# Optimization experiments

Hardware: AMD Instinct MI355X
Metric: run time of the kernel (lower is better)

## Reference

```python
import jax, jax.numpy as jnp
import numpy as np

S, B, D = 2048, 32, 1024
H = 16
DIM = D // H  # 64 per-head dim
EPS = 1e-5


def setup_inputs() -> dict:
    key = jax.random.key(0)
    k1, k2, k3 = jax.random.split(key, 3)
    src = jax.random.normal(k1, (S, B, D), dtype=jnp.float32)
    # per-head bracket Linear(2*dim -> dim), stacked over heads
    bound = 1.0 / np.sqrt(2 * DIM)
    W = jax.random.uniform(k2, (H, 2 * DIM, DIM), minval=-bound, maxval=bound, dtype=jnp.float32)
    b = jax.random.uniform(k3, (H, DIM), minval=-bound, maxval=bound, dtype=jnp.float32)
    # shared LayerNorm(d_model) params (default init: gamma=1, beta=0)
    gamma = jnp.ones((D,), dtype=jnp.float32)
    beta = jnp.zeros((D,), dtype=jnp.float32)
    return {"src": src, "W": W, "b": b, "gamma": gamma, "beta": beta}


def reference(src, W, b, gamma, beta):
    def layer_norm(x):
        mu = jnp.mean(x, axis=-1, keepdims=True)
        var = jnp.mean(jnp.square(x - mu), axis=-1, keepdims=True)
        return (x - mu) * jax.lax.rsqrt(var + EPS) * gamma + beta

    def step(c, x):
        # c, x: [B, D]; mode='base': y_h = GELU(Linear_h([c_h; x_h])), new context = x
        ch = c.reshape(B, H, DIM)
        xh = x.reshape(B, H, DIM)
        cat = jnp.concatenate([ch, xh], axis=-1)              # [B, H, 2*DIM]
        y = jax.nn.gelu(jnp.einsum('bhk,hkd->bhd', cat, W) + b, approximate=False)
        c_new = layer_norm(x)                                  # LN(context)=LN(x)
        y_out = layer_norm(y.reshape(B, D))
        return c_new, y_out

    c0 = jnp.zeros((B, D), dtype=src.dtype)
    _, ys = jax.lax.scan(step, c0, src)
    return ys  # [S, B, D]
```

## Files before the change

### kernel.cpp

```cpp
#include <hip/hip_runtime.h>

#define SS 2048
#define BB 32
#define DD 1024
#define HH 16
#define RB 8

typedef unsigned short u16;
typedef unsigned int u32;
using f32x4 = __attribute__((ext_vector_type(4))) float;
using bf16x8 = __attribute__((ext_vector_type(8))) short;

__device__ __forceinline__ u16 f2bf(float x) {
  union { float f; u32 u; } c; c.f = x;
  u32 r = c.u + 0x7fffu + ((c.u >> 16) & 1u);
  return (u16)(r >> 16);
}
__device__ __forceinline__ int swzb(int row, int col) {
  return ((row << 11) + (col << 1)) ^ ((row & 7) << 4);
}
__device__ __forceinline__ void st_lds8(u16* base, int row, int col,
                                        float4 a, float4 b) {
  uint4 pk;
  pk.x = (u32)f2bf(a.x) | ((u32)f2bf(a.y) << 16);
  pk.y = (u32)f2bf(a.z) | ((u32)f2bf(a.w) << 16);
  pk.z = (u32)f2bf(b.x) | ((u32)f2bf(b.y) << 16);
  pk.w = (u32)f2bf(b.z) | ((u32)f2bf(b.w) << 16);
  *reinterpret_cast<uint4*>(reinterpret_cast<char*>(base) + swzb(row, col)) = pk;
}
__device__ __forceinline__ void st_lds8z(u16* base, int row, int col) {
  uint4 pk; pk.x = pk.y = pk.z = pk.w = 0u;
  *reinterpret_cast<uint4*>(reinterpret_cast<char*>(base) + swzb(row, col)) = pk;
}
__device__ __forceinline__ bf16x8 ld_afrag(const u16* base, int row, int col) {
  return *reinterpret_cast<const bf16x8*>(reinterpret_cast<const char*>(base) + swzb(row, col));
}
__device__ __forceinline__ float gelu_f(float v) {
  const float u2 = 1.5957691216057308f * v * __builtin_fmaf(0.044715f, v * v, 1.0f);
  const float e = __expf(u2);
  const float th = 1.0f - 2.0f * __builtin_amdgcn_rcpf(e + 1.0f);
  return 0.5f * v * (1.0f + th);
}

__global__ void prep_w(const float* __restrict__ W, u16* __restrict__ Wf) {
  const int o = blockIdx.x * 256 + threadIdx.x;
  const int l = o & 63;
  const int tile = o >> 6;
  const int nt = tile & 3, ks = (tile >> 2) & 3, h = tile >> 4;
  const int d = nt * 16 + (l & 15);
  const int kb = ks * 32 + 8 * (l >> 4);
  u16 v[8];
#pragma unroll
  for (int j = 0; j < 8; ++j) v[j] = f2bf(W[(h * 128 + kb + j) * 64 + d]);
  uint4 pk;
  pk.x = (u32)v[0] | ((u32)v[1] << 16);
  pk.y = (u32)v[2] | ((u32)v[3] << 16);
  pk.z = (u32)v[4] | ((u32)v[5] << 16);
  pk.w = (u32)v[6] | ((u32)v[7] << 16);
  reinterpret_cast<uint4*>(Wf)[o] = pk;
}

__global__ __launch_bounds__(256, 4) void lienet_main(
    const float* __restrict__ src, const u16* __restrict__ Wf,
    const float* __restrict__ bias, const float* __restrict__ gamma,
    const float* __restrict__ beta, float* __restrict__ out) {
  __shared__ __align__(16) u16 cbuf[RB * DD];
  __shared__ __align__(16) u16 xbuf[RB * DD];
  __shared__ float part[4][RB][2];

  const int bid = blockIdx.x;
  const int lin = (bid & 7) * 1024 + (bid >> 3);
  const int t = lin >> 2;
  const int row0 = (lin & 3) * RB;

  const int tid = threadIdx.x;
  const int wave = tid >> 6;
  const int lane = tid & 63;
  const int c0 = lane * 8;

#pragma unroll
  for (int rr = 0; rr < 2; ++rr) {
    const int row = wave * 2 + rr;
    const int grow = row0 + row;
    {
      const float* rp = src + ((size_t)t * BB + grow) * DD;
      float4 f0 = *reinterpret_cast<const float4*>(rp + c0);
      float4 f1 = *reinterpret_cast<const float4*>(rp + c0 + 4);
      float4 f2 = *reinterpret_cast<const float4*>(rp + 512 + c0);
      float4 f3 = *reinterpret_cast<const float4*>(rp + 512 + c0 + 4);
      st_lds8(xbuf, row, c0, f0, f1);
      st_lds8(xbuf, row, 512 + c0, f2, f3);
    }
    if (t == 0) {
      st_lds8z(cbuf, row, c0);
      st_lds8z(cbuf, row, 512 + c0);
    } else {
      const float* rp = src + ((size_t)(t - 1) * BB + grow) * DD;
      float f[16];
      *reinterpret_cast<float4*>(f + 0) = *reinterpret_cast<const float4*>(rp + c0);
      *reinterpret_cast<float4*>(f + 4) = *reinterpret_cast<const float4*>(rp + c0 + 4);
      *reinterpret_cast<float4*>(f + 8) = *reinterpret_cast<const float4*>(rp + 512 + c0);
      *reinterpret_cast<float4*>(f + 12) = *reinterpret_cast<const float4*>(rp + 512 + c0 + 4);
      float s1 = 0.f, s2 = 0.f;
#pragma unroll
      for (int j = 0; j < 16; ++j) { s1 += f[j]; s2 += f[j] * f[j]; }
#pragma unroll
      for (int off = 32; off; off >>= 1) { s1 += __shfl_xor(s1, off); s2 += __shfl_xor(s2, off); }
      const float mu = s1 * (1.f / 1024.f);
      const float rs = rsqrtf(s2 * (1.f / 1024.f) - mu * mu + 1e-5f);
      float4 g0 = *reinterpret_cast<const float4*>(gamma + c0);
      float4 g1 = *reinterpret_cast<const float4*>(gamma + c0 + 4);
      float4 g2 = *reinterpret_cast<const float4*>(gamma + 512 + c0);
      float4 g3 = *reinterpret_cast<const float4*>(gamma + 512 + c0 + 4);
      float4 b0 = *reinterpret_cast<const float4*>(beta + c0);
      float4 b1 = *reinterpret_cast<const float4*>(beta + c0 + 4);
      float4 b2 = *reinterpret_cast<const float4*>(beta + 512 + c0);
      float4 b3 = *reinterpret_cast<const float4*>(beta + 512 + c0 + 4);
      float4 o0, o1, o2, o3;
      o0.x = (f[0] - mu) * rs * g0.x + b0.x;  o0.y = (f[1] - mu) * rs * g0.y + b0.y;
      o0.z = (f[2] - mu) * rs * g0.z + b0.z;  o0.w = (f[3] - mu) * rs * g0.w + b0.w;
      o1.x = (f[4] - mu) * rs * g1.x + b1.x;  o1.y = (f[5] - mu) * rs * g1.y + b1.y;
      o1.z = (f[6] - mu) * rs * g1.z + b1.z;  o1.w = (f[7] - mu) * rs * g1.w + b1.w;
      o2.x = (f[8] - mu) * rs * g2.x + b2.x;  o2.y = (f[9] - mu) * rs * g2.y + b2.y;
      o2.z = (f[10] - mu) * rs * g2.z + b2.z; o2.w = (f[11] - mu) * rs * g2.w + b2.w;
      o3.x = (f[12] - mu) * rs * g3.x + b3.x; o3.y = (f[13] - mu) * rs * g3.y + b3.y;
      o3.z = (f[14] - mu) * rs * g3.z + b3.z; o3.w = (f[15] - mu) * rs * g3.w + b3.w;
      st_lds8(cbuf, row, c0, o0, o1);
      st_lds8(cbuf, row, 512 + c0, o2, o3);
    }
  }
  __syncthreads();

  f32x4 acc[4][4];
#pragma unroll
  for (int hh = 0; hh < 4; ++hh)
#pragma unroll
    for (int nt = 0; nt < 4; ++nt) acc[hh][nt] = (f32x4){0.f, 0.f, 0.f, 0.f};

  const int arow = lane & 7;
  const int kb = 8 * (lane >> 4);
#pragma unroll
  for (int ks = 0; ks < 4; ++ks) {
    const u16* sb = (ks < 2) ? cbuf : xbuf;
#pragma unroll
    for (int hh = 0; hh < 4; ++hh) {
      const int h = wave * 4 + hh;
      bf16x8 a = ld_afrag(sb, arow, h * 64 + (ks & 1) * 32 + kb);
      const uint4* wp = reinterpret_cast<const uint4*>(Wf) + ((h * 4 + ks) * 4) * 64 + lane;
#pragma unroll
      for (int nt = 0; nt < 4; ++nt) {
        uint4 wv = wp[nt * 64];
        bf16x8 bfr = *reinterpret_cast<bf16x8*>(&wv);
        acc[hh][nt] = __builtin_amdgcn_mfma_f32_16x16x32_bf16(a, bfr, acc[hh][nt], 0, 0, 0);
      }
    }
  }

  const int hilo = lane >> 5;
  const int row4 = 4 * ((lane >> 4) & 1);
  const int cl = lane & 15;
  float gv[2][4][4];
#pragma unroll
  for (int hp = 0; hp < 2; ++hp) {
    const int h_eff = wave * 4 + hp + 2 * hilo;
#pragma unroll
    for (int nt = 0; nt < 4; ++nt) {
      const float bv = bias[h_eff * 64 + nt * 16 + cl];
#pragma unroll
      for (int r = 0; r < 4; ++r) {
        const float v = (hilo ? acc[hp + 2][nt][r] : acc[hp][nt][r]) + bv;
        gv[hp][nt][r] = gelu_f(v);
      }
    }
  }
  float s1[4], s2[4];
#pragma unroll
  for (int r = 0; r < 4; ++r) {
    float a = 0.f, b = 0.f;
#pragma unroll
    for (int hp = 0; hp < 2; ++hp)
#pragma unroll
      for (int nt = 0; nt < 4; ++nt) {
        const float g = gv[hp][nt][r];
        a += g; b += g * g;
      }
    a += __shfl_xor(a, 1); b += __shfl_xor(b, 1);
    a += __shfl_xor(a, 2); b += __shfl_xor(b, 2);
    a += __shfl_xor(a, 4); b += __shfl_xor(b, 4);
    a += __shfl_xor(a, 8); b += __shfl_xor(b, 8);
    a += __shfl_xor(a, 32); b += __shfl_xor(b, 32);
    s1[r] = a; s2[r] = b;
  }
  if (lane == 0 || lane == 16) {
#pragma unroll
    for (int r = 0; r < 4; ++r) {
      part[wave][row4 + r][0] = s1[r];
      part[wave][row4 + r][1] = s2[r];
    }
  }
  float gm[2][4], bt[2][4];
#pragma unroll
  for (int hp = 0; hp < 2; ++hp) {
    const int h_eff = wave * 4 + hp + 2 * hilo;
#pragma unroll
    for (int nt = 0; nt < 4; ++nt) {
      const int dcol = h_eff * 64 + nt * 16 + cl;
      gm[hp][nt] = gamma[dcol];
      bt[hp][nt] = beta[dcol];
    }
  }
  __syncthreads();

  float mu[4], rs[4];
#pragma unroll
  for (int r = 0; r < 4; ++r) {
    const int row = row4 + r;
    const float a = part[0][row][0] + part[1][row][0] + part[2][row][0] + part[3][row][0];
    const float b = part[0][row][1] + part[1][row][1] + part[2][row][1] + part[3][row][1];
    mu[r] = a * (1.f / 1024.f);
    rs[r] = rsqrtf(b * (1.f / 1024.f) - mu[r] * mu[r] + 1e-5f);
  }
#pragma unroll
  for (int hp = 0; hp < 2; ++hp) {
    const int h_eff = wave * 4 + hp + 2 * hilo;
#pragma unroll
    for (int nt = 0; nt < 4; ++nt) {
      const int dcol = h_eff * 64 + nt * 16 + cl;
#pragma unroll
      for (int r = 0; r < 4; ++r) {
        const float o = (gv[hp][nt][r] - mu[r]) * rs[r] * gm[hp][nt] + bt[hp][nt];
        out[((size_t)t * BB + row0 + row4 + r) * DD + dcol] = o;
      }
    }
  }
}

extern "C" void kernel_launch(void* const* d_in, const int* in_sizes, int n_in,
                              void* d_out, int out_size, void* d_ws, size_t ws_size,
                              hipStream_t stream) {
  const float* src = (const float*)d_in[0];
  const float* W = (const float*)d_in[1];
  const float* bias = (const float*)d_in[2];
  const float* gamma = (const float*)d_in[3];
  const float* beta = (const float*)d_in[4];
  float* out = (float*)d_out;
  u16* Wf = (u16*)d_ws;

  prep_w<<<64, 256, 0, stream>>>(W, Wf);
  lienet_main<<<SS * 4, 256, 0, stream>>>(src, Wf, bias, gamma, beta, out);
}
```

Baseline: 228.4 us.

## Process eight timesteps per block, reusing the staged input as next context

Each block now loops over eight consecutive timesteps for sixteen batch rows with 512 threads. The LDS copy of x for step t is turned in place into the LayerNorm context for step t+1, and the next x is prefetched into registers while GELU and the reductions run. This removes the second global read of src for the context and fills all sixteen MFMA rows instead of eight. In exchange the grid shrinks to 512 larger blocks with serial steps and extra barriers. The context LayerNorm is now computed from bf16-rounded x rather than fp32, which slightly changes numerics.

```diff
diff --git a/kernel.cpp b/kernel.cpp
--- a/kernel.cpp
+++ b/kernel.cpp
@@ -3,8 +3,9 @@
 #define SS 2048
 #define BB 32
 #define DD 1024
-#define HH 16
-#define RB 8
+#define RB 16
+#define GT 8
+#define NW 8
 
 typedef unsigned short u16;
 typedef unsigned int u32;
@@ -16,11 +17,13 @@
   u32 r = c.u + 0x7fffu + ((c.u >> 16) & 1u);
   return (u16)(r >> 16);
 }
+__device__ __forceinline__ float bf2f(u32 h) {
+  union { u32 u; float f; } c; c.u = h << 16; return c.f;
+}
 __device__ __forceinline__ int swzb(int row, int col) {
   return ((row << 11) + (col << 1)) ^ ((row & 7) << 4);
 }
-__device__ __forceinline__ void st_lds8(u16* base, int row, int col,
-                                        float4 a, float4 b) {
+__device__ __forceinline__ void st8(u16* base, int row, int col, float4 a, float4 b) {
   uint4 pk;
   pk.x = (u32)f2bf(a.x) | ((u32)f2bf(a.y) << 16);
   pk.y = (u32)f2bf(a.z) | ((u32)f2bf(a.w) << 16);
@@ -28,9 +31,12 @@
   pk.w = (u32)f2bf(b.z) | ((u32)f2bf(b.w) << 16);
   *reinterpret_cast<uint4*>(reinterpret_cast<char*>(base) + swzb(row, col)) = pk;
 }
-__device__ __forceinline__ void st_lds8z(u16* base, int row, int col) {
+__device__ __forceinline__ void st8z(u16* base, int row, int col) {
   uint4 pk; pk.x = pk.y = pk.z = pk.w = 0u;
   *reinterpret_cast<uint4*>(reinterpret_cast<char*>(base) + swzb(row, col)) = pk;
+}
+__device__ __forceinline__ uint4 ld16(const u16* base, int row, int col) {
+  return *reinterpret_cast<const uint4*>(reinterpret_cast<const char*>(base) + swzb(row, col));
 }
 __device__ __forceinline__ bf16x8 ld_afrag(const u16* base, int row, int col) {
   return *reinterpret_cast<const bf16x8*>(reinterpret_cast<const char*>(base) + swzb(row, col));
@@ -40,6 +46,37 @@
   const float e = __expf(u2);
   const float th = 1.0f - 2.0f * __builtin_amdgcn_rcpf(e + 1.0f);
   return 0.5f * v * (1.0f + th);
+}
+
+__device__ __forceinline__ void ln_row_to_c(u16* cbuf, int row, int c0, const float* v,
+                                            const float* __restrict__ gamma,
+                                            const float* __restrict__ beta) {
+  float s1 = 0.f, s2 = 0.f;
+#pragma unroll
+  for (int j = 0; j < 16; ++j) { s1 += v[j]; s2 += v[j] * v[j]; }
+#pragma unroll
+  for (int off = 32; off; off >>= 1) { s1 += __shfl_xor(s1, off); s2 += __shfl_xor(s2, off); }
+  const float mu = s1 * (1.f / 1024.f);
+  const float rs = rsqrtf(s2 * (1.f / 1024.f) - mu * mu + 1e-5f);
+  float4 g0 = *reinterpret_cast<const float4*>(gamma + c0);
+  float4 g1 = *reinterpret_cast<const float4*>(gamma + c0 + 4);
+  float4 g2 = *reinterpret_cast<const float4*>(gamma + 512 + c0);
+  float4 g3 = *reinterpret_cast<const float4*>(gamma + 512 + c0 + 4);
+  float4 b0 = *reinterpret_cast<const float4*>(beta + c0);
+  float4 b1 = *reinterpret_cast<const float4*>(beta + c0 + 4);
+  float4 b2 = *reinterpret_cast<const float4*>(beta + 512 + c0);
+  float4 b3 = *reinterpret_cast<const float4*>(beta + 512 + c0 + 4);
+  float4 o0, o1, o2, o3;
+  o0.x = (v[0] - mu) * rs * g0.x + b0.x;   o0.y = (v[1] - mu) * rs * g0.y + b0.y;
+  o0.z = (v[2] - mu) * rs * g0.z + b0.z;   o0.w = (v[3] - mu) * rs * g0.w + b0.w;
+  o1.x = (v[4] - mu) * rs * g1.x + b1.x;   o1.y = (v[5] - mu) * rs * g1.y + b1.y;
+  o1.z = (v[6] - mu) * rs * g1.z + b1.z;   o1.w = (v[7] - mu) * rs * g1.w + b1.w;
+  o2.x = (v[8] - mu) * rs * g2.x + b2.x;   o2.y = (v[9] - mu) * rs * g2.y + b2.y;
+  o2.z = (v[10] - mu) * rs * g2.z + b2.z;  o2.w = (v[11] - mu) * rs * g2.w + b2.w;
+  o3.x = (v[12] - mu) * rs * g3.x + b3.x;  o3.y = (v[13] - mu) * rs * g3.y + b3.y;
+  o3.z = (v[14] - mu) * rs * g3.z + b3.z;  o3.w = (v[15] - mu) * rs * g3.w + b3.w;
+  st8(cbuf, row, c0, o0, o1);
+  st8(cbuf, row, 512 + c0, o2, o3);
 }
 
 __global__ void prep_w(const float* __restrict__ W, u16* __restrict__ Wf) {
@@ -48,10 +85,10 @@
   const int tile = o >> 6;
   const int nt = tile & 3, ks = (tile >> 2) & 3, h = tile >> 4;
   const int d = nt * 16 + (l & 15);
-  const int kb = ks * 32 + 8 * (l >> 4);
+  const int kbw = ks * 32 + 8 * (l >> 4);
   u16 v[8];
 #pragma unroll
-  for (int j = 0; j < 8; ++j) v[j] = f2bf(W[(h * 128 + kb + j) * 64 + d]);
+  for (int j = 0; j < 8; ++j) v[j] = f2bf(W[(h * 128 + kbw + j) * 64 + d]);
   uint4 pk;
   pk.x = (u32)v[0] | ((u32)v[1] << 16);
   pk.y = (u32)v[2] | ((u32)v[3] << 16);
@@ -60,178 +97,162 @@
   reinterpret_cast<uint4*>(Wf)[o] = pk;
 }
 
-__global__ __launch_bounds__(256, 4) void lienet_main(
+__global__ __launch_bounds__(512, 4) void lienet_main(
     const float* __restrict__ src, const u16* __restrict__ Wf,
     const float* __restrict__ bias, const float* __restrict__ gamma,
     const float* __restrict__ beta, float* __restrict__ out) {
   __shared__ __align__(16) u16 cbuf[RB * DD];
   __shared__ __align__(16) u16 xbuf[RB * DD];
-  __shared__ float part[4][RB][2];
+  __shared__ __align__(16) float part[RB][NW][2];
 
   const int bid = blockIdx.x;
-  const int lin = (bid & 7) * 1024 + (bid >> 3);
-  const int t = lin >> 2;
-  const int row0 = (lin & 3) * RB;
+  const int t0 = (bid >> 1) * GT;
+  const int rg = bid & 1;
 
   const int tid = threadIdx.x;
   const int wave = tid >> 6;
   const int lane = tid & 63;
   const int c0 = lane * 8;
+  const int r0 = wave * 2;
+  const int kb = 8 * (lane >> 4);
+  const int cl = lane & 15;
+  const int rq = lane >> 4;
 
 #pragma unroll
   for (int rr = 0; rr < 2; ++rr) {
-    const int row = wave * 2 + rr;
-    const int grow = row0 + row;
-    {
-      const float* rp = src + ((size_t)t * BB + grow) * DD;
-      float4 f0 = *reinterpret_cast<const float4*>(rp + c0);
-      float4 f1 = *reinterpret_cast<const float4*>(rp + c0 + 4);
-      float4 f2 = *reinterpret_cast<const float4*>(rp + 512 + c0);
-      float4 f3 = *reinterpret_cast<const float4*>(rp + 512 + c0 + 4);
-      st_lds8(xbuf, row, c0, f0, f1);
-      st_lds8(xbuf, row, 512 + c0, f2, f3);
-    }
-    if (t == 0) {
-      st_lds8z(cbuf, row, c0);
-      st_lds8z(cbuf, row, 512 + c0);
+    const int row = r0 + rr;
+    const int grow = rg * RB + row;
+    const float* xp = src + ((size_t)t0 * BB + grow) * DD;
+    float4 xa = *reinterpret_cast<const float4*>(xp + c0);
+    float4 xb = *reinterpret_cast<const float4*>(xp + c0 + 4);
+    float4 xc = *reinterpret_cast<const float4*>(xp + 512 + c0);
+    float4 xd = *reinterpret_cast<const float4*>(xp + 512 + c0 + 4);
+    st8(xbuf, row, c0, xa, xb);
+    st8(xbuf, row, 512 + c0, xc, xd);
+    if (t0 == 0) {
+      st8z(cbuf, row, c0);
+      st8z(cbuf, row, 512 + c0);
     } else {
-      const float* rp = src + ((size_t)(t - 1) * BB + grow) * DD;
-      float f[16];
-      *reinterpret_cast<float4*>(f + 0) = *reinterpret_cast<const float4*>(rp + c0);
-      *reinterpret_cast<float4*>(f + 4) = *reinterpret_cast<const float4*>(rp + c0 + 4);
-      *reinterpret_cast<float4*>(f + 8) = *reinterpret_cast<const float4*>(rp + 512 + c0);
-      *reinterpret_cast<float4*>(f + 12) = *reinterpret_cast<const float4*>(rp + 512 + c0 + 4);
-      float s1 = 0.f, s2 = 0.f;
-#pragma unroll
-      for (int j = 0; j < 16; ++j) { s1 += f[j]; s2 += f[j] * f[j]; }
-#pragma unroll
-      for (int off = 32; off; off >>= 1) { s1 += __shfl_xor(s1, off); s2 += __shfl_xor(s2, off); }
-      const float mu = s1 * (1.f / 1024.f);
-      const float rs = rsqrtf(s2 * (1.f / 1024.f) - mu * mu + 1e-5f);
-      float4 g0 = *reinterpret_cast<const float4*>(gamma + c0);
-      float4 g1 = *reinterpret_cast<const float4*>(gamma + c0 + 4);
-      float4 g2 = *reinterpret_cast<const float4*>(gamma + 512 + c0);
-      float4 g3 = *reinterpret_cast<const float4*>(gamma + 512 + c0 + 4);
-      float4 b0 = *reinterpret_cast<const float4*>(beta + c0);
-      float4 b1 = *reinterpret_cast<const float4*>(beta + c0 + 4);
-      float4 b2 = *reinterpret_cast<const float4*>(beta + 512 + c0);
-      float4 b3 = *reinterpret_cast<const float4*>(beta + 512 + c0 + 4);
-      float4 o0, o1, o2, o3;
-      o0.x = (f[0] - mu) * rs * g0.x + b0.x;  o0.y = (f[1] - mu) * rs * g0.y + b0.y;
-      o0.z = (f[2] - mu) * rs * g0.z + b0.z;  o0.w = (f[3] - mu) * rs * g0.w + b0.w;
-      o1.x = (f[4] - mu) * rs * g1.x + b1.x;  o1.y = (f[5] - mu) * rs * g1.y + b1.y;
-      o1.z = (f[6] - mu) * rs * g1.z + b1.z;  o1.w = (f[7] - mu) * rs * g1.w + b1.w;
-      o2.x = (f[8] - mu) * rs * g2.x + b2.x;  o2.y = (f[9] - mu) * rs * g2.y + b2.y;
-      o2.z = (f[10] - mu) * rs * g2.z + b2.z; o2.w = (f[11] - mu) * rs * g2.w + b2.w;
-      o3.x = (f[12] - mu) * rs * g3.x + b3.x; o3.y = (f[13] - mu) * rs * g3.y + b3.y;
-      o3.z = (f[14] - mu) * rs * g3.z + b3.z; o3.w = (f[15] - mu) * rs * g3.w + b3.w;
-      st_lds8(cbuf, row, c0, o0, o1);
-      st_lds8(cbuf, row, 512 + c0, o2, o3);
+      const float* cp = src + ((size_t)(t0 - 1) * BB + grow) * DD;
+      float v[16];
+      *reinterpret_cast<float4*>(v + 0)  = *reinterpret_cast<const float4*>(cp + c0);
+      *reinterpret_cast<float4*>(v + 4)  = *reinterpret_cast<const float4*>(cp + c0 + 4);
+      *reinterpret_cast<float4*>(v + 8)  = *reinterpret_cast<const float4*>(cp + 512 + c0);
+      *reinterpret_cast<float4*>(v + 12) = *reinterpret_cast<const float4*>(cp + 512 + c0 + 4);
+      ln_row_to_c(cbuf, row, c0, v, gamma, beta);
     }
   }
+  f32x4 acc[2][4];
+#pragma unroll
+  for (int hh = 0; hh < 2; ++hh)
+#pragma unroll
+    for (int nt = 0; nt < 4; ++nt) acc[hh][nt] = (f32x4){0.f, 0.f, 0.f, 0.f};
   __syncthreads();
 
-  f32x4 acc[4][4];
-#pragma unroll
-  for (int hh = 0; hh < 4; ++hh)
-#pragma unroll
-    for (int nt = 0; nt < 4; ++nt) acc[hh][nt] = (f32x4){0.f, 0.f, 0.f, 0.f};
-
-  const int arow = lane & 7;
-  const int kb = 8 * (lane >> 4);
-#pragma unroll
-  for (int ks = 0; ks < 4; ++ks) {
-    const u16* sb = (ks < 2) ? cbuf : xbuf;
-#pragma unroll
-    for (int hh = 0; hh < 4; ++hh) {
-      const int h = wave * 4 + hh;
-      bf16x8 a = ld_afrag(sb, arow, h * 64 + (ks & 1) * 32 + kb);
-      const uint4* wp = reinterpret_cast<const uint4*>(Wf) + ((h * 4 + ks) * 4) * 64 + lane;
+  for (int t = t0; t < t0 + GT; ++t) {
+    __builtin_amdgcn_s_setprio(1);
+#pragma unroll
+    for (int ks = 0; ks < 4; ++ks) {
+      const u16* sb = (ks < 2) ? cbuf : xbuf;
+#pragma unroll
+      for (int hh = 0; hh < 2; ++hh) {
+        const int h = wave * 2 + hh;
+        bf16x8 afr = ld_afrag(sb, cl, h * 64 + (ks & 1) * 32 + kb);
+        const uint4* wp = reinterpret_cast<const uint4*>(Wf) + ((h * 4 + ks) * 4) * 64 + lane;
+#pragma unroll
+        for (int nt = 0; nt < 4; ++nt) {
+          uint4 wv = wp[nt * 64];
+          bf16x8 bfr = *reinterpret_cast<bf16x8*>(&wv);
+          acc[hh][nt] = __builtin_amdgcn_mfma_f32_16x16x32_bf16(afr, bfr, acc[hh][nt], 0, 0, 0);
+        }
+      }
+    }
+    __builtin_amdgcn_s_setprio(0);
+
+    const bool stage = (t + 1 < t0 + GT);
+    float4 nx[2][4];
+    if (stage) {
+#pragma unroll
+      for (int rr = 0; rr < 2; ++rr) {
+        const float* xp = src + ((size_t)(t + 1) * BB + rg * RB + r0 + rr) * DD;
+        nx[rr][0] = *reinterpret_cast<const float4*>(xp + c0);
+        nx[rr][1] = *reinterpret_cast<const float4*>(xp + c0 + 4);
+        nx[rr][2] = *reinterpret_cast<const float4*>(xp + 512 + c0);
+        nx[rr][3] = *reinterpret_cast<const float4*>(xp + 512 + c0 + 4);
+      }
+    }
+#pragma unroll
+    for (int hh = 0; hh < 2; ++hh)
 #pragma unroll
       for (int nt = 0; nt < 4; ++nt) {
-        uint4 wv = wp[nt * 64];
-        bf16x8 bfr = *reinterpret_cast<bf16x8*>(&wv);
-        acc[hh][nt] = __builtin_amdgcn_mfma_f32_16x16x32_bf16(a, bfr, acc[hh][nt], 0, 0, 0);
-      }
-    }
-  }
-
-  const int hilo = lane >> 5;
-  const int row4 = 4 * ((lane >> 4) & 1);
-  const int cl = lane & 15;
-  float gv[2][4][4];
-#pragma unroll
-  for (int hp = 0; hp < 2; ++hp) {
-    const int h_eff = wave * 4 + hp + 2 * hilo;
-#pragma unroll
-    for (int nt = 0; nt < 4; ++nt) {
-      const float bv = bias[h_eff * 64 + nt * 16 + cl];
-#pragma unroll
-      for (int r = 0; r < 4; ++r) {
-        const float v = (hilo ? acc[hp + 2][nt][r] : acc[hp][nt][r]) + bv;
-        gv[hp][nt][r] = gelu_f(v);
-      }
-    }
-  }
-  float s1[4], s2[4];
-#pragma unroll
-  for (int r = 0; r < 4; ++r) {
-    float a = 0.f, b = 0.f;
-#pragma unroll
-    for (int hp = 0; hp < 2; ++hp)
+        const float bv = bias[(wave * 2 + hh) * 64 + nt * 16 + cl];
+#pragma unroll
+        for (int r = 0; r < 4; ++r)
+          acc[hh][nt][r] = gelu_f(acc[hh][nt][r] + bv);
+      }
+#pragma unroll
+    for (int r = 0; r < 4; ++r) {
+      float a = 0.f, b = 0.f;
+#pragma unroll
+      for (int hh = 0; hh < 2; ++hh)
+#pragma unroll
+        for (int nt = 0; nt < 4; ++nt) {
+          const float g = acc[hh][nt][r];
+          a += g; b += g * g;
+        }
+      a += __shfl_xor(a, 1); b += __shfl_xor(b, 1);
+      a += __shfl_xor(a, 2); b += __shfl_xor(b, 2);
+      a += __shfl_xor(a, 4); b += __shfl_xor(b, 4);
+      a += __shfl_xor(a, 8); b += __shfl_xor(b, 8);
+      if (cl == 0) { part[rq * 4 + r][wave][0] = a; part[rq * 4 + r][wave][1] = b; }
+    }
+    __syncthreads();
+
+    if (stage) {
+#pragma unroll
+      for (int rr = 0; rr < 2; ++rr) {
+        const int row = r0 + rr;
+        uint4 g0 = ld16(xbuf, row, c0);
+        uint4 g1 = ld16(xbuf, row, 512 + c0);
+        float v[16];
+        v[0] = bf2f(g0.x & 0xffffu);  v[1] = bf2f(g0.x >> 16);
+        v[2] = bf2f(g0.y & 0xffffu);  v[3] = bf2f(g0.y >> 16);
+        v[4] = bf2f(g0.z & 0xffffu);  v[5] = bf2f(g0.z >> 16);
+        v[6] = bf2f(g0.w & 0xffffu);  v[7] = bf2f(g0.w >> 16);
+        v[8] = bf2f(g1.x & 0xffffu);  v[9] = bf2f(g1.x >> 16);
+        v[10] = bf2f(g1.y & 0xffffu); v[11] = bf2f(g1.y >> 16);
+        v[12] = bf2f(g1.z & 0xffffu); v[13] = bf2f(g1.z >> 16);
+        v[14] = bf2f(g1.w & 0xffffu); v[15] = bf2f(g1.w >> 16);
+        ln_row_to_c(cbuf, row, c0, v, gamma, beta);
+        st8(xbuf, row, c0, nx[rr][0], nx[rr][1]);
+        st8(xbuf, row, 512 + c0, nx[rr][2], nx[rr][3]);
+      }
+    }
+
+    float mu[4], rs[4];
+#pragma unroll
+    for (int r = 0; r < 4; ++r) {
+      const float4* pp = reinterpret_cast<const float4*>(&part[rq * 4 + r][0][0]);
+      float4 p0 = pp[0], p1 = pp[1], p2 = pp[2], p3 = pp[3];
+      const float a = p0.x + p0.z + p1.x + p1.z + p2.x + p2.z + p3.x + p3.z;
+      const float b = p0.y + p0.w + p1.y + p1.w + p2.y + p2.w + p3.y + p3.w;
+      mu[r] = a * (1.f / 1024.f);
+      rs[r] = rsqrtf(b * (1.f / 1024.f) - mu[r] * mu[r] + 1e-5f);
+    }
+#pragma unroll
+    for (int hh = 0; hh < 2; ++hh)
 #pragma unroll
       for (int nt = 0; nt < 4; ++nt) {
-        const float g = gv[hp][nt][r];
-        a += g; b += g * g;
-      }
-    a += __shfl_xor(a, 1); b += __shfl_xor(b, 1);
-    a += __shfl_xor(a, 2); b += __shfl_xor(b, 2);
-    a += __shfl_xor(a, 4); b += __shfl_xor(b, 4);
-    a += __shfl_xor(a, 8); b += __shfl_xor(b, 8);
-    a += __shfl_xor(a, 32); b += __shfl_xor(b, 32);
-    s1[r] = a; s2[r] = b;
-  }
-  if (lane == 0 || lane == 16) {
-#pragma unroll
-    for (int r = 0; r < 4; ++r) {
-      part[wave][row4 + r][0] = s1[r];
-      part[wave][row4 + r][1] = s2[r];
-    }
-  }
-  float gm[2][4], bt[2][4];
-#pragma unroll
-  for (int hp = 0; hp < 2; ++hp) {
-    const int h_eff = wave * 4 + hp + 2 * hilo;
-#pragma unroll
-    for (int nt = 0; nt < 4; ++nt) {
-      const int dcol = h_eff * 64 + nt * 16 + cl;
-      gm[hp][nt] = gamma[dcol];
-      bt[hp][nt] = beta[dcol];
-    }
-  }
-  __syncthreads();
-
-  float mu[4], rs[4];
-#pragma unroll
-  for (int r = 0; r < 4; ++r) {
-    const int row = row4 + r;
-    const float a = part[0][row][0] + part[1][row][0] + part[2][row][0] + part[3][row][0];
-    const float b = part[0][row][1] + part[1][row][1] + part[2][row][1] + part[3][row][1];
-    mu[r] = a * (1.f / 1024.f);
-    rs[r] = rsqrtf(b * (1.f / 1024.f) - mu[r] * mu[r] + 1e-5f);
-  }
-#pragma unroll
-  for (int hp = 0; hp < 2; ++hp) {
-    const int h_eff = wave * 4 + hp + 2 * hilo;
-#pragma unroll
-    for (int nt = 0; nt < 4; ++nt) {
-      const int dcol = h_eff * 64 + nt * 16 + cl;
-#pragma unroll
-      for (int r = 0; r < 4; ++r) {
-        const float o = (gv[hp][nt][r] - mu[r]) * rs[r] * gm[hp][nt] + bt[hp][nt];
-        out[((size_t)t * BB + row0 + row4 + r) * DD + dcol] = o;
-      }
-    }
+        const int dcol = (wave * 2 + hh) * 64 + nt * 16 + cl;
+        const float eg = gamma[dcol], eb = beta[dcol];
+#pragma unroll
+        for (int r = 0; r < 4; ++r) {
+          out[((size_t)t * BB + rg * RB + rq * 4 + r) * DD + dcol] =
+              (acc[hh][nt][r] - mu[r]) * rs[r] * eg + eb;
+          acc[hh][nt][r] = 0.f;
+        }
+      }
+    __syncthreads();
   }
 }
 
@@ -247,5 +268,5 @@
   u16* Wf = (u16*)d_ws;
 
   prep_w<<<64, 256, 0, stream>>>(W, Wf);
-  lienet_main<<<SS * 4, 256, 0, stream>>>(src, Wf, bias, gamma, beta, out);
-}
+  lienet_main<<<(SS / GT) * 2, 512, 0, stream>>>(src, Wf, bias, gamma, beta, out);
+}
```

After: 620.1 us. +171.6%, slower.
